# Performance work log

Measured on AMD Instinct MI355X. Metric: run time of the kernel, lower is better.

Reference implementation:

```python
import jax, jax.numpy as jnp
from jax import lax
import numpy as np

B, C_IN, C_OUT, H, W = 4, 256, 256, 64, 64
P = 4
DM = C_IN // P            # 64, d_model per parallel chunk
D_STATE = 16
D_CONV = 4
EXPAND = 2
D_INNER = EXPAND * DM     # 128
DT_RANK = max(1, -(-DM // 16))  # ceil(64/16) = 4


def setup_inputs() -> dict:
    key = jax.random.key(0)
    ks = jax.random.split(key, 12)
    s = lambda k, shape, scale=0.02: (jax.random.normal(k, shape, jnp.float32) * scale)
    dt = jax.random.uniform(ks[5], (D_INNER,), jnp.float32, 1e-3, 0.1)
    dt_bias = jnp.log(jnp.expm1(dt))  # inverse softplus, as in mamba_ssm init
    A_log = jnp.log(jnp.tile(jnp.arange(1, D_STATE + 1, dtype=jnp.float32), (D_INNER, 1)))
    return {
        "x": jax.random.normal(ks[0], (B, C_IN, H, W), jnp.float32),
        "ln_g": jnp.ones((C_IN,), jnp.float32),
        "ln_b": jnp.zeros((C_IN,), jnp.float32),
        "in_proj_w": s(ks[1], (2 * D_INNER, DM)),
        "conv_w": s(ks[2], (D_INNER, D_CONV), 0.1),
        "conv_b": jnp.zeros((D_INNER,), jnp.float32),
        "x_proj_w": s(ks[3], (DT_RANK + 2 * D_STATE, D_INNER)),
        "dt_proj_w": s(ks[4], (D_INNER, DT_RANK), 0.1),
        "dt_proj_b": dt_bias,
        "A_log": A_log,
        "D": jnp.ones((D_INNER,), jnp.float32),
        "out_proj_w": s(ks[6], (DM, D_INNER)),
        "skip_scale": jnp.ones((1,), jnp.float32),
        "proj_w": s(ks[7], (C_OUT, C_IN)),
        "proj_b": jnp.zeros((C_OUT,), jnp.float32),
        "cdc_w": s(ks[8], (C_OUT, 1, 3, 3), 0.1),      # depthwise 3x3, groups=C_OUT
        "theta_w": jnp.zeros((1, C_OUT), jnp.float32),  # nn.init.constant_(weight, 0)
        "theta_b": jnp.full((1,), -2.0, jnp.float32),   # nn.init.constant_(bias, -2)
        "pw_w": s(ks[9], (C_OUT, C_OUT)),               # 1x1 pointwise conv, no bias
    }


def _layernorm(x, g, b, eps=1e-5):
    mu = x.mean(-1, keepdims=True)
    var = ((x - mu) ** 2).mean(-1, keepdims=True)
    return (x - mu) * lax.rsqrt(var + eps) * g + b


def _mamba(x, in_proj_w, conv_w, conv_b, x_proj_w, dt_proj_w, dt_proj_b, A_log, D, out_proj_w):
    # x: [Bm, L, DM]
    xz = jnp.einsum('bld,ed->ble', x, in_proj_w)          # [Bm, L, 2*D_INNER]
    xc, z = jnp.split(xz, 2, axis=-1)
    # causal depthwise conv1d along L
    xt = jnp.swapaxes(xc, 1, 2)                           # [Bm, D_INNER, L]
    xt = lax.conv_general_dilated(xt, conv_w[:, None, :], (1,), [(D_CONV - 1, 0)],
                                  dimension_numbers=('NCH', 'OIH', 'NCH'),
                                  feature_group_count=D_INNER)
    xt = xt + conv_b[None, :, None]
    xs = jax.nn.silu(jnp.swapaxes(xt, 1, 2))              # [Bm, L, D_INNER]
    x_dbl = jnp.einsum('bld,ed->ble', xs, x_proj_w)       # [Bm, L, DT_RANK+2*D_STATE]
    dt, Bmat, Cmat = jnp.split(x_dbl, [DT_RANK, DT_RANK + D_STATE], axis=-1)
    delta = jax.nn.softplus(jnp.einsum('blr,dr->bld', dt, dt_proj_w) + dt_proj_b)
    A = -jnp.exp(A_log)                                   # [D_INNER, D_STATE]

    def step(h, inp):
        d_t, b_t, c_t, u_t = inp                          # [Bm,di],[Bm,ds],[Bm,ds],[Bm,di]
        h = h * jnp.exp(d_t[..., None] * A) + (d_t * u_t)[..., None] * b_t[:, None, :]
        return h, jnp.einsum('bds,bs->bd', h, c_t)

    h0 = jnp.zeros((x.shape[0], D_INNER, D_STATE), x.dtype)
    xs_t = (jnp.swapaxes(delta, 0, 1), jnp.swapaxes(Bmat, 0, 1),
            jnp.swapaxes(Cmat, 0, 1), jnp.swapaxes(xs, 0, 1))
    _, ys = lax.scan(step, h0, xs_t)                      # ys: [L, Bm, D_INNER]
    y = jnp.swapaxes(ys, 0, 1) + xs * D
    y = y * jax.nn.silu(z)
    return jnp.einsum('bld,od->blo', y, out_proj_w)       # [Bm, L, DM]


def reference(x, ln_g, ln_b, in_proj_w, conv_w, conv_b, x_proj_w, dt_proj_w, dt_proj_b,
              A_log, D, out_proj_w, skip_scale, proj_w, proj_b, cdc_w, theta_w, theta_b, pw_w):
    Bb, C = x.shape[:2]
    Hh, Ww = x.shape[2], x.shape[3]
    L = Hh * Ww
    x_flat = jnp.swapaxes(x.reshape(Bb, C, L), 1, 2)      # [B, L, C]
    x_norm = _layernorm(x_flat, ln_g, ln_b)
    # chunk along channel dim into P pieces, run shared Mamba on all as one big batch
    xc = jnp.moveaxis(x_norm.reshape(Bb, L, P, DM), 2, 0).reshape(P * Bb, L, DM)
    ym = _mamba(xc, in_proj_w, conv_w, conv_b, x_proj_w, dt_proj_w, dt_proj_b,
                A_log, D, out_proj_w) + skip_scale * xc
    ym = jnp.moveaxis(ym.reshape(P, Bb, L, DM), 0, 2).reshape(Bb, L, C)
    ym = _layernorm(ym, ln_g, ln_b)                       # same norm params (shared)
    yp = jnp.einsum('blc,oc->blo', ym, proj_w) + proj_b
    out = jnp.swapaxes(yp, 1, 2).reshape(Bb, C_OUT, Hh, Ww)
    # A_CDC: depthwise 3x3 conv + central-difference term
    out_normal = lax.conv_general_dilated(out, cdc_w, (1, 1), [(1, 1), (1, 1)],
                                          dimension_numbers=('NCHW', 'OIHW', 'NCHW'),
                                          feature_group_count=C_OUT)
    ksum = cdc_w.sum(axis=(2, 3))[:, 0]                   # [C_OUT]; depthwise 1x1 == scale
    edge = out_normal - out * ksum[None, :, None, None]
    theta = jax.nn.sigmoid(jnp.einsum('bchw,oc->bohw', out, theta_w)
                           + theta_b[None, :, None, None])
    cdc_out = out_normal + theta * edge
    g = jax.nn.gelu(cdc_out, approximate=False)           # nn.GELU exact
    cnn_out = jnp.einsum('bchw,oc->bohw', g, pw_w)        # 1x1 conv, no bias
    return out + cnn_out
```

## Files before the change

kernel.cpp:

```cpp
#include <hip/hip_runtime.h>
#include <hip/hip_bf16.h>
#include <math.h>

typedef __hip_bfloat16 bf16;
typedef short bf8_t __attribute__((ext_vector_type(8)));
typedef float f4_t  __attribute__((ext_vector_type(4)));
typedef float f2_t  __attribute__((ext_vector_type(2)));
#define MFMA16(a,b,c) __builtin_amdgcn_mfma_f32_16x16x32_bf16(a,b,c,0,0,0)
#define DEV __device__ __forceinline__

DEV float bf2f(bf16 h){ return __bfloat162float(h); }
DEV bf16 f2bf(float f){ return __float2bfloat16(f); }
DEV float ld(const void* p, size_t i, int md){
  return md ? ((const float*)p)[i] : bf2f(((const bf16*)p)[i]);
}
DEV float wred(float v){
  #pragma unroll
  for(int off=32; off>0; off>>=1) v += __shfl_down(v, off, 64);
  return __shfl(v, 0, 64);
}

__global__ __launch_bounds__(256) void k_detect(const unsigned short* __restrict__ xr, int* __restrict__ flag){
  __shared__ float sm[4];
  int t = threadIdx.x;
  float m = 0.f;
  for(int i=t;i<8192;i+=256){
    unsigned int w = ((unsigned int)xr[i]) << 16;
    float v = fabsf(__uint_as_float(w));
    if(v != v) v = 1e30f;
    m = fmaxf(m, v);
  }
  #pragma unroll
  for(int off=32; off>0; off>>=1) m = fmaxf(m, __shfl_down(m, off, 64));
  if((t & 63) == 0) sm[t >> 6] = m;
  __syncthreads();
  if(t == 0){
    float mm = fmaxf(fmaxf(sm[0], sm[1]), fmaxf(sm[2], sm[3]));
    *flag = (mm > 1e10f) ? 1 : 0;
  }
}

__global__ __launch_bounds__(256) void k_wcvt(const void* __restrict__ inw, const void* __restrict__ outw,
                                              const void* __restrict__ projw, const void* __restrict__ pww,
                                              bf16* __restrict__ dst, const int* __restrict__ modep){
  const int md = *modep;
  int g = blockIdx.x*256 + threadIdx.x;
  if(g >= 155648) return;
  const void* src; int i;
  if(g < 16384){ src = inw;   i = g; }
  else if(g < 24576){ src = outw;  i = g - 16384; }
  else if(g < 90112){ src = projw; i = g - 24576; }
  else { src = pww; i = g - 90112; }
  dst[g] = f2bf(ld(src, (size_t)i, md));
}

__global__ __launch_bounds__(256) void k_ln1(const void* __restrict__ x, const void* __restrict__ gam,
                                             const void* __restrict__ bet, bf16* __restrict__ xnb,
                                             const int* __restrict__ modep){
  __shared__ float sh[64*257];
  __shared__ float mus[64], rss[64];
  const int md = *modep;
  int t = threadIdx.x;
  int b = blockIdx.x >> 6, lt = blockIdx.x & 63;
  int l0 = lt << 6;
  int lane = t & 63, cg = t >> 6;
  size_t xbase = ((size_t)b << 20) + l0 + lane;
  if(md){
    const float* xp = (const float*)x + xbase;
    #pragma unroll 8
    for(int c = cg; c < 256; c += 4)
      sh[lane*257 + c] = xp[(size_t)c << 12];
  } else {
    const bf16* xp = (const bf16*)x + xbase;
    #pragma unroll 8
    for(int c = cg; c < 256; c += 4)
      sh[lane*257 + c] = bf2f(xp[(size_t)c << 12]);
  }
  __syncthreads();
  {
    int row = t >> 2, q = t & 3;
    const float* rp = sh + row*257 + q*64;
    float s = 0.f, s2 = 0.f;
    #pragma unroll 8
    for(int i=0;i<64;i++){ float v = rp[i]; s += v; s2 += v*v; }
    s  += __shfl_xor(s, 1, 64);  s2 += __shfl_xor(s2, 1, 64);
    s  += __shfl_xor(s, 2, 64);  s2 += __shfl_xor(s2, 2, 64);
    if(q == 0){
      float mu = s*(1.f/256.f);
      mus[row] = mu;
      rss[row] = rsqrtf(s2*(1.f/256.f) - mu*mu + 1e-5f);
    }
  }
  __syncthreads();
  int r0 = (t >> 6) << 4;
  #pragma unroll
  for(int k=0;k<4;k++){
    int c = (t & 63) + (k << 6);
    float gv = ld(gam, c, md), bv = ld(bet, c, md);
    #pragma unroll 4
    for(int rr=0; rr<16; rr++){
      int row = r0 + rr;
      xnb[((size_t)(b*4096 + l0 + row))*256 + c] =
        f2bf((sh[row*257 + c] - mus[row])*rss[row]*gv + bv);
    }
  }
}

__global__ __launch_bounds__(256) void k_inproj(const bf16* __restrict__ xnb, const bf16* __restrict__ wb,
                                                bf16* __restrict__ xcb, bf16* __restrict__ zb){
  __shared__ bf16 As[64*72];
  __shared__ bf16 Ws[256*72];
  int t = threadIdx.x;
  int bm = blockIdx.x >> 6, lt = blockIdx.x & 63;
  int p = bm >> 2, b = bm & 3, l0 = lt << 6;
  #pragma unroll
  for(int pass=0; pass<2; pass++){
    int idx = t + pass*256, r = idx >> 3, ch = idx & 7;
    *(uint4*)&As[r*72 + ch*8] = *(const uint4*)&xnb[((size_t)(b*4096 + l0 + r))*256 + p*64 + ch*8];
  }
  #pragma unroll
  for(int pass=0; pass<8; pass++){
    int idx = t + pass*256, e = idx >> 3, ch = idx & 7;
    *(uint4*)&Ws[e*72 + ch*8] = *(const uint4*)&wb[(size_t)e*64 + ch*8];
  }
  __syncthreads();
  int lane = t & 63, w = t >> 6, quad = lane >> 4, lr = lane & 15;
  f4_t acc[16];
  #pragma unroll
  for(int nt=0;nt<16;nt++) acc[nt] = (f4_t){0.f,0.f,0.f,0.f};
  #pragma unroll
  for(int kk=0; kk<64; kk+=32){
    bf8_t a = *(const bf8_t*)&As[(w*16 + lr)*72 + kk + quad*8];
    #pragma unroll
    for(int nt=0;nt<16;nt++){
      bf8_t bb = *(const bf8_t*)&Ws[(nt*16 + lr)*72 + kk + quad*8];
      acc[nt] = MFMA16(a, bb, acc[nt]);
    }
  }
  __syncthreads();
  bf16* Sl = Ws;
  #pragma unroll
  for(int nt=0;nt<16;nt++)
    #pragma unroll
    for(int r=0;r<4;r++)
      Sl[(w*16 + quad*4 + r)*264 + nt*16 + lr] = f2bf(acc[nt][r]);
  __syncthreads();
  #pragma unroll
  for(int pass=0; pass<8; pass++){
    int idx = t + pass*256, l = idx >> 5, c16 = idx & 31;
    int e0 = c16*8;
    uint4 v = *(uint4*)&Sl[l*264 + e0];
    size_t row = (size_t)bm*4096 + l0 + l;
    if(e0 < 128) *(uint4*)&xcb[row*128 + e0] = v;
    else         *(uint4*)&zb[row*128 + e0 - 128] = v;
  }
}

__global__ __launch_bounds__(256) void k_conv(const bf16* __restrict__ xcb, const void* __restrict__ cw,
                                              const void* __restrict__ cb, bf16* __restrict__ xsb,
                                              const int* __restrict__ modep){
  const int md = *modep;
  int g = blockIdx.x*256 + threadIdx.x;
  int d = g & 127;
  int t4 = g >> 7;
  int l4 = t4 & 1023;
  int bm = t4 >> 10;
  int l0 = l4 << 2;
  size_t base = ((size_t)bm*4096 + l0)*128 + d;
  const bf16* p = xcb + base;
  float w0 = ld(cw,(size_t)(d<<2)+0,md), w1 = ld(cw,(size_t)(d<<2)+1,md);
  float w2 = ld(cw,(size_t)(d<<2)+2,md), w3 = ld(cw,(size_t)(d<<2)+3,md);
  float bv = ld(cb,(size_t)d,md);
  float xm3, xm2, xm1;
  if(l4 > 0){ xm3 = bf2f(p[-384]); xm2 = bf2f(p[-256]); xm1 = bf2f(p[-128]); }
  else      { xm3 = 0.f; xm2 = 0.f; xm1 = 0.f; }
  float x0 = bf2f(p[0]), x1 = bf2f(p[128]), x2 = bf2f(p[256]), x3 = bf2f(p[384]);
  float y0 = fmaf(w0,xm3, fmaf(w1,xm2, fmaf(w2,xm1, fmaf(w3,x0, bv))));
  float y1 = fmaf(w0,xm2, fmaf(w1,xm1, fmaf(w2,x0,  fmaf(w3,x1, bv))));
  float y2 = fmaf(w0,xm1, fmaf(w1,x0,  fmaf(w2,x1,  fmaf(w3,x2, bv))));
  float y3 = fmaf(w0,x0,  fmaf(w1,x1,  fmaf(w2,x2,  fmaf(w3,x3, bv))));
  bf16* o = xsb + base;
  o[0]   = f2bf(y0 / (1.f + __expf(-y0)));
  o[128] = f2bf(y1 / (1.f + __expf(-y1)));
  o[256] = f2bf(y2 / (1.f + __expf(-y2)));
  o[384] = f2bf(y3 / (1.f + __expf(-y3)));
}

__global__ __launch_bounds__(256) void k_xproj(const bf16* __restrict__ xsb, const void* __restrict__ w,
                                               float* __restrict__ xdbl, const int* __restrict__ modep){
  __shared__ float At[128*68];
  __shared__ float Ww[128*40];
  const int md = *modep;
  int t = threadIdx.x;
  int bm = blockIdx.x >> 6, lt = blockIdx.x & 63, l0 = lt << 6;
  for(int idx = t; idx < 4608; idx += 256){
    int e = idx >> 7, k = idx & 127;
    Ww[k*40 + e] = ld(w, idx, md);
  }
  for(int idx = t; idx < 8192; idx += 256){
    int l = idx >> 7, k = idx & 127;
    At[k*68 + l] = bf2f(xsb[((size_t)bm*4096 + l0 + l)*128 + k]);
  }
  __syncthreads();
  int l = t & 63, eg = t >> 6;
  float acc[9] = {};
  for(int k=0;k<128;k++){
    float a = At[k*68 + l];
    #pragma unroll
    for(int j=0;j<9;j++) acc[j] = fmaf(a, Ww[k*40 + eg*9 + j], acc[j]);
  }
  float* o = xdbl + ((size_t)bm*4096 + l0 + l)*36 + eg*9;
  #pragma unroll
  for(int j=0;j<9;j++) o[j] = acc[j];
}

#define PTREE2(P, e1) \
  float e2s=(e1)*(e1), e4s=e2s*e2s, e8s=e4s*e4s; \
  f2_t P##0={(e1),e2s}; \
  f2_t P##1=P##0*(f2_t){e2s,e2s}; \
  f2_t e4v_={e4s,e4s}; f2_t P##2=P##0*e4v_, P##3=P##1*e4v_; \
  f2_t e8v_={e8s,e8s}; f2_t P##4=P##0*e8v_, P##5=P##1*e8v_, P##6=P##2*e8v_, P##7=P##3*e8v_;

__global__ __launch_bounds__(128) void k_scan1(const bf16* __restrict__ xsb, const float* __restrict__ xdbl,
                                               const void* __restrict__ dtw, const void* __restrict__ dtb,
                                               const void* __restrict__ Alog,
                                               float* __restrict__ CP, bf16* __restrict__ CSb,
                                               const int* __restrict__ modep){
  __shared__ float sh[32*36];
  __shared__ bf16 su[32*128];
  const int md = *modep;
  int d = threadIdx.x;
  int bm = blockIdx.x >> 7, c = blockIdx.x & 127;
  size_t row0 = (size_t)bm*4096 + (c<<5);
  {
    const float4* src = (const float4*)(xdbl + row0*36);
    for(int idx = d; idx < 288; idx += 128) ((float4*)sh)[idx] = src[idx];
    const uint4* gu = (const uint4*)(xsb + row0*128);
    uint4* lu = (uint4*)su;
    #pragma unroll
    for(int j=0;j<4;j++) lu[d + j*128] = gu[d + j*128];
  }
  float A[16];
  #pragma unroll
  for(int s=0;s<16;s++) A[s] = -expf(ld(Alog, (size_t)((d<<4)+s), md));
  float A0 = A[0];
  int fastf = 1;
  #pragma unroll
  for(int s=0;s<16;s++){
    float n = (float)(s+1);
    if(fabsf(A[s] - n*A0) > 2e-3f*fabsf(n*A0)) fastf = 0;
  }
  fastf = __all(fastf);
  float wdt[4];
  #pragma unroll
  for(int j=0;j<4;j++) wdt[j] = ld(dtw, (size_t)((d<<2)+j), md);
  float bdt = ld(dtb, (size_t)d, md);
  __syncthreads();
  f2_t h2[8];
  #pragma unroll
  for(int j=0;j<8;j++) h2[j] = (f2_t){0.f,0.f};
  float sumd = 0.f;
  if(fastf){
    #pragma unroll
    for(int tt=0;tt<32;tt++){
      const float* r = sh + tt*36;
      float4 dt4 = *(const float4*)r;
      float v = fmaf(dt4.x,wdt[0], fmaf(dt4.y,wdt[1], fmaf(dt4.z,wdt[2], fmaf(dt4.w,wdt[3], bdt))));
      float dv = fmaxf(v,0.f) + __logf(1.f + __expf(-fabsf(v)));
      float u = bf2f(su[tt*128 + d]);
      float du = dv*u; sumd += dv;
      const f2_t* B2 = (const f2_t*)(r+4);
      float e1 = __expf(dv*A0);
      PTREE2(p, e1);
      f2_t du2 = {du,du};
      h2[0] = h2[0]*p0 + du2*B2[0];
      h2[1] = h2[1]*p1 + du2*B2[1];
      h2[2] = h2[2]*p2 + du2*B2[2];
      h2[3] = h2[3]*p3 + du2*B2[3];
      h2[4] = h2[4]*p4 + du2*B2[4];
      h2[5] = h2[5]*p5 + du2*B2[5];
      h2[6] = h2[6]*p6 + du2*B2[6];
      h2[7] = h2[7]*p7 + du2*B2[7];
    }
  } else {
    for(int tt=0;tt<32;tt++){
      const float* r = sh + tt*36;
      float4 dt4 = *(const float4*)r;
      float v = fmaf(dt4.x,wdt[0], fmaf(dt4.y,wdt[1], fmaf(dt4.z,wdt[2], fmaf(dt4.w,wdt[3], bdt))));
      float dv = fmaxf(v,0.f) + __logf(1.f + __expf(-fabsf(v)));
      float u = bf2f(su[tt*128 + d]);
      float du = dv*u; sumd += dv;
      const float* Bp = r + 4;
      #pragma unroll
      for(int j=0;j<8;j++){
        f2_t e = { __expf(dv*A[2*j]), __expf(dv*A[2*j+1]) };
        f2_t bb = { Bp[2*j], Bp[2*j+1] };
        h2[j] = h2[j]*e + (f2_t){du,du}*bb;
      }
    }
  }
  size_t ob = ((size_t)(bm*128 + c)*128 + d) << 4;
  if(fastf){
    float qv = __expf(sumd*A0);
    PTREE2(P, qv);
    *(f2_t*)&CP[ob+ 0]=P0; *(f2_t*)&CP[ob+ 2]=P1; *(f2_t*)&CP[ob+ 4]=P2; *(f2_t*)&CP[ob+ 6]=P3;
    *(f2_t*)&CP[ob+ 8]=P4; *(f2_t*)&CP[ob+10]=P5; *(f2_t*)&CP[ob+12]=P6; *(f2_t*)&CP[ob+14]=P7;
  } else {
    #pragma unroll
    for(int s=0;s<16;s++) CP[ob+s] = __expf(sumd*A[s]);
  }
  __align__(16) bf16 pk[8];
  #pragma unroll
  for(int j=0;j<4;j++){ pk[2*j] = f2bf(h2[j].x); pk[2*j+1] = f2bf(h2[j].y); }
  *(uint4*)&CSb[ob] = *(uint4*)pk;
  #pragma unroll
  for(int j=0;j<4;j++){ pk[2*j] = f2bf(h2[4+j].x); pk[2*j+1] = f2bf(h2[4+j].y); }
  *(uint4*)&CSb[ob+8] = *(uint4*)pk;
}

__global__ __launch_bounds__(64) void k_scan2(float* __restrict__ CP, const bf16* __restrict__ CSb){
  int g = blockIdx.x*64 + threadIdx.x;
  int bm = g >> 11, ds = g & 2047;
  size_t base = ((size_t)bm << 18) + ds;
  float Pb[8], Sb[8];
  #pragma unroll
  for(int j=0;j<8;j++){
    size_t idx = base + ((size_t)j << 11);
    Pb[j] = CP[idx]; Sb[j] = bf2f(CSb[idx]);
  }
  float h = 0.f;
  #pragma unroll
  for(int grp=0; grp<16; grp++){
    float Pc[8], Sc[8];
    #pragma unroll
    for(int j=0;j<8;j++){ Pc[j]=Pb[j]; Sc[j]=Sb[j]; }
    if(grp < 15){
      #pragma unroll
      for(int j=0;j<8;j++){
        size_t idx = base + ((size_t)((grp+1)*8 + j) << 11);
        Pb[j] = CP[idx]; Sb[j] = bf2f(CSb[idx]);
      }
    }
    #pragma unroll
    for(int j=0;j<8;j++){
      size_t idx = base + ((size_t)(grp*8 + j) << 11);
      CP[idx] = h;
      h = fmaf(Pc[j], h, Sc[j]);
    }
  }
}

__global__ __launch_bounds__(128) void k_scan3(bf16* __restrict__ zb, const bf16* __restrict__ xsb,
                                               const float* __restrict__ xdbl,
                                               const void* __restrict__ dtw, const void* __restrict__ dtb,
                                               const void* __restrict__ Alog, const void* __restrict__ Dw,
                                               const float* __restrict__ CP, const int* __restrict__ modep){
  __shared__ float sh[32*36];
  __shared__ bf16 su[32*128];
  const int md = *modep;
  int d = threadIdx.x;
  int bm = blockIdx.x >> 7, c = blockIdx.x & 127;
  size_t row0 = (size_t)bm*4096 + (c<<5);
  {
    const float4* src = (const float4*)(xdbl + row0*36);
    for(int idx = d; idx < 288; idx += 128) ((float4*)sh)[idx] = src[idx];
    const uint4* gu = (const uint4*)(xsb + row0*128);
    uint4* lu = (uint4*)su;
    #pragma unroll
    for(int j=0;j<4;j++) lu[d + j*128] = gu[d + j*128];
  }
  float A[16];
  #pragma unroll
  for(int s=0;s<16;s++) A[s] = -expf(ld(Alog, (size_t)((d<<4)+s), md));
  float A0 = A[0];
  int fastf = 1;
  #pragma unroll
  for(int s=0;s<16;s++){
    float n = (float)(s+1);
    if(fabsf(A[s] - n*A0) > 2e-3f*fabsf(n*A0)) fastf = 0;
  }
  fastf = __all(fastf);
  float wdt[4];
  #pragma unroll
  for(int j=0;j<4;j++) wdt[j] = ld(dtw, (size_t)((d<<2)+j), md);
  float bdt = ld(dtb, (size_t)d, md);
  float Dd = ld(Dw, (size_t)d, md);
  size_t hb = ((size_t)(bm*128 + c)*128 + d) << 4;
  f2_t h2[8];
  #pragma unroll
  for(int j=0;j<8;j++) h2[j] = *(const f2_t*)&CP[hb + 2*j];
  __syncthreads();
  if(fastf){
    #pragma unroll
    for(int tt=0;tt<32;tt++){
      const float* r = sh + tt*36;
      size_t bg = (row0 + tt)*128 + d;
      float zv = bf2f(zb[bg]);
      float4 dt4 = *(const float4*)r;
      float v = fmaf(dt4.x,wdt[0], fmaf(dt4.y,wdt[1], fmaf(dt4.z,wdt[2], fmaf(dt4.w,wdt[3], bdt))));
      float dv = fmaxf(v,0.f) + __logf(1.f + __expf(-fabsf(v)));
      float u  = bf2f(su[tt*128 + d]);
      float du = dv*u;
      const f2_t* B2 = (const f2_t*)(r+4);
      const f2_t* C2 = (const f2_t*)(r+20);
      float e1 = __expf(dv*A0);
      PTREE2(p, e1);
      f2_t du2 = {du,du};
      f2_t ya = {0.f,0.f}, yb = {0.f,0.f};
      h2[0] = h2[0]*p0 + du2*B2[0];  ya += h2[0]*C2[0];
      h2[1] = h2[1]*p1 + du2*B2[1];  yb += h2[1]*C2[1];
      h2[2] = h2[2]*p2 + du2*B2[2];  ya += h2[2]*C2[2];
      h2[3] = h2[3]*p3 + du2*B2[3];  yb += h2[3]*C2[3];
      h2[4] = h2[4]*p4 + du2*B2[4];  ya += h2[4]*C2[4];
      h2[5] = h2[5]*p5 + du2*B2[5];  yb += h2[5]*C2[5];
      h2[6] = h2[6]*p6 + du2*B2[6];  ya += h2[6]*C2[6];
      h2[7] = h2[7]*p7 + du2*B2[7];  yb += h2[7]*C2[7];
      float y = (ya.x + ya.y) + (yb.x + yb.y);
      float yv = (y + u*Dd) * (zv / (1.f + __expf(-zv)));
      zb[bg] = f2bf(yv);
    }
  } else {
    for(int tt=0;tt<32;tt++){
      const float* r = sh + tt*36;
      size_t bg = (row0 + tt)*128 + d;
      float zv = bf2f(zb[bg]);
      float4 dt4 = *(const float4*)r;
      float v = fmaf(dt4.x,wdt[0], fmaf(dt4.y,wdt[1], fmaf(dt4.z,wdt[2], fmaf(dt4.w,wdt[3], bdt))));
      float dv = fmaxf(v,0.f) + __logf(1.f + __expf(-fabsf(v)));
      float u  = bf2f(su[tt*128 + d]);
      float du = dv*u;
      const float* Bp = r + 4;
      const float* Cp = r + 20;
      f2_t ya = {0.f,0.f};
      #pragma unroll
      for(int j=0;j<8;j++){
        f2_t e = { __expf(dv*A[2*j]), __expf(dv*A[2*j+1]) };
        f2_t bb = { Bp[2*j], Bp[2*j+1] };
        f2_t cc = { Cp[2*j], Cp[2*j+1] };
        h2[j] = h2[j]*e + (f2_t){du,du}*bb;
        ya += h2[j]*cc;
      }
      float y = ya.x + ya.y;
      float yv = (y + u*Dd) * (zv / (1.f + __expf(-zv)));
      zb[bg] = f2bf(yv);
    }
  }
}

__global__ __launch_bounds__(256) void k_outproj(const bf16* __restrict__ yb, const bf16* __restrict__ xnb,
                                                 const bf16* __restrict__ wb, const void* __restrict__ ss,
                                                 bf16* __restrict__ ymb, const int* __restrict__ modep){
  __shared__ bf16 As[64*72];
  __shared__ bf16 Ws[64*72];
  const int md = *modep;
  int t = threadIdx.x;
  int bm = blockIdx.x >> 6, lt = blockIdx.x & 63;
  int p = bm >> 2, b = bm & 3, l0 = lt << 6;
  int lane = t & 63, w = t >> 6, quad = lane >> 4, lr = lane & 15;
  f4_t acc[4];
  #pragma unroll
  for(int nt=0;nt<4;nt++) acc[nt] = (f4_t){0.f,0.f,0.f,0.f};
  for(int kb=0; kb<2; kb++){
    if(kb) __syncthreads();
    int k0 = kb << 6;
    #pragma unroll
    for(int pass=0; pass<2; pass++){
      int idx = t + pass*256, r = idx >> 3, ch = idx & 7;
      *(uint4*)&As[r*72 + ch*8] = *(const uint4*)&yb[((size_t)bm*4096 + l0 + r)*128 + k0 + ch*8];
    }
    #pragma unroll
    for(int pass=0; pass<2; pass++){
      int idx = t + pass*256, o = idx >> 3, ch = idx & 7;
      *(uint4*)&Ws[o*72 + ch*8] = *(const uint4*)&wb[(size_t)o*128 + k0 + ch*8];
    }
    __syncthreads();
    #pragma unroll
    for(int kk=0; kk<64; kk+=32){
      bf8_t a = *(const bf8_t*)&As[(w*16 + lr)*72 + kk + quad*8];
      #pragma unroll
      for(int nt=0;nt<4;nt++){
        bf8_t bb = *(const bf8_t*)&Ws[(nt*16 + lr)*72 + kk + quad*8];
        acc[nt] = MFMA16(a, bb, acc[nt]);
      }
    }
  }
  __syncthreads();
  bf16* Sl = As;
  #pragma unroll
  for(int nt=0;nt<4;nt++)
    #pragma unroll
    for(int r=0;r<4;r++)
      Sl[(w*16 + quad*4 + r)*72 + nt*16 + lr] = f2bf(acc[nt][r]);
  __syncthreads();
  float sv = ld(ss, 0, md);
  #pragma unroll
  for(int pass=0; pass<2; pass++){
    int idx = t + pass*256, l = idx >> 3, ch = idx & 7;
    size_t gi = ((size_t)b*4096 + l0 + l)*256 + p*64 + ch*8;
    uint4 yv = *(uint4*)&Sl[l*72 + ch*8];
    uint4 xv = *(const uint4*)&xnb[gi];
    const bf16* y8 = (const bf16*)&yv;
    const bf16* x8 = (const bf16*)&xv;
    uint4 ov; bf16* o8 = (bf16*)&ov;
    #pragma unroll
    for(int j=0;j<8;j++) o8[j] = f2bf(fmaf(sv, bf2f(x8[j]), bf2f(y8[j])));
    *(uint4*)&ymb[gi] = ov;
  }
}

__global__ __launch_bounds__(256) void k_ln2(bf16* __restrict__ ymb, const void* __restrict__ gam,
                                             const void* __restrict__ bet, const int* __restrict__ modep){
  const int md = *modep;
  int lane = threadIdx.x & 63, wv = threadIdx.x >> 6;
  size_t row = (size_t)blockIdx.x*4 + wv;
  bf16* rp = ymb + row*256 + (lane<<2);
  __align__(8) bf16 raw[4];
  *(ushort4*)raw = *(const ushort4*)rp;
  float v[4];
  #pragma unroll
  for(int i=0;i<4;i++) v[i] = bf2f(raw[i]);
  float s = v[0]+v[1]+v[2]+v[3];
  float s2 = v[0]*v[0]+v[1]*v[1]+v[2]*v[2]+v[3]*v[3];
  s = wred(s); s2 = wred(s2);
  float mu = s*(1.f/256.f);
  float rs = rsqrtf(s2*(1.f/256.f) - mu*mu + 1e-5f);
  int c = lane << 2;
  #pragma unroll
  for(int i=0;i<4;i++) raw[i] = f2bf((v[i]-mu)*rs*ld(gam,c+i,md) + ld(bet,c+i,md));
  *(ushort4*)rp = *(ushort4*)raw;
}

__global__ __launch_bounds__(256) void k_proj(const bf16* __restrict__ ymb, const bf16* __restrict__ wb,
                                              const void* __restrict__ pb, bf16* __restrict__ outbb,
                                              const void* __restrict__ tw, const void* __restrict__ tb2,
                                              float* __restrict__ theta, const int* __restrict__ modep){
  __shared__ bf16 As[64*72];
  __shared__ bf16 Ws[256*72];
  const int md = *modep;
  int t = threadIdx.x;
  int row0 = blockIdx.x << 6;
  int b = row0 >> 12, l0 = row0 & 4095;
  int lane = t & 63, w = t >> 6, quad = lane >> 4, lr = lane & 15;
  f4_t acc[16];
  #pragma unroll
  for(int nt=0;nt<16;nt++) acc[nt] = (f4_t){0.f,0.f,0.f,0.f};
  for(int kb=0; kb<4; kb++){
    if(kb) __syncthreads();
    int k0 = kb << 6;
    #pragma unroll
    for(int pass=0; pass<2; pass++){
      int idx = t + pass*256, r = idx >> 3, ch = idx & 7;
      *(uint4*)&As[r*72 + ch*8] = *(const uint4*)&ymb[((size_t)(row0 + r))*256 + k0 + ch*8];
    }
    #pragma unroll
    for(int pass=0; pass<8; pass++){
      int idx = t + pass*256, e = idx >> 3, ch = idx & 7;
      *(uint4*)&Ws[e*72 + ch*8] = *(const uint4*)&wb[(size_t)e*256 + k0 + ch*8];
    }
    __syncthreads();
    #pragma unroll
    for(int kk=0; kk<64; kk+=32){
      bf8_t a = *(const bf8_t*)&As[(w*16 + lr)*72 + kk + quad*8];
      #pragma unroll
      for(int nt=0;nt<16;nt++){
        bf8_t bb = *(const bf8_t*)&Ws[(nt*16 + lr)*72 + kk + quad*8];
        acc[nt] = MFMA16(a, bb, acc[nt]);
      }
    }
  }
  __syncthreads();
  bf16* Sl = Ws;
  #pragma unroll
  for(int nt=0;nt<16;nt++){
    float bv = ld(pb, nt*16 + lr, md);
    #pragma unroll
    for(int r=0;r<4;r++)
      Sl[(nt*16 + lr)*72 + w*16 + quad*4 + r] = f2bf(acc[nt][r] + bv);
  }
  __syncthreads();
  #pragma unroll
  for(int pass=0; pass<8; pass++){
    int idx = t + pass*256, o = idx >> 3, ch = idx & 7;
    uint4 v = *(uint4*)&Sl[o*72 + ch*8];
    *(uint4*)&outbb[((size_t)(b*256 + o) << 12) + l0 + ch*8] = v;
  }
  if(t < 64){
    float acc2 = 0.f;
    #pragma unroll 8
    for(int o=0;o<256;o++)
      acc2 = fmaf(bf2f(Sl[o*72 + t]), ld(tw, (size_t)o, md), acc2);
    float v = acc2 + ld(tb2, 0, md);
    theta[((size_t)b << 12) + l0 + t] = 1.f / (1.f + __expf(-v));
  }
}

__global__ __launch_bounds__(256) void k_cdc(const bf16* __restrict__ outbb, const float* __restrict__ theta,
                                             const void* __restrict__ cw, bf16* __restrict__ gbufb,
                                             const int* __restrict__ modep){
  const int md = *modep;
  int g = blockIdx.x*256 + threadIdx.x;
  int w4 = g & 15;
  int h0 = (g >> 4) & 63;
  int c  = (g >> 10) & 255;
  int b  = g >> 18;
  int w0 = w4 << 2;
  float wk[9]; float ks = 0.f;
  #pragma unroll
  for(int j=0;j<9;j++){ wk[j] = ld(cw, (size_t)c*9 + j, md); ks += wk[j]; }
  const bf16* base = outbb + (((size_t)b*256 + c) << 12);
  float X[3][6];
  #pragma unroll
  for(int dy=0;dy<3;dy++){
    int hh = h0 + dy - 1;
    #pragma unroll
    for(int dx=0;dx<6;dx++){
      int ww = w0 + dx - 1;
      X[dy][dx] = (hh>=0 && hh<64 && ww>=0 && ww<64) ? bf2f(base[(hh<<6)+ww]) : 0.f;
    }
  }
  float4 th = *(const float4*)&theta[((size_t)b<<12) + (h0<<6) + w0];
  float thv[4] = {th.x, th.y, th.z, th.w};
  __align__(8) bf16 outp[4];
  #pragma unroll
  for(int k=0;k<4;k++){
    float on = 0.f;
    #pragma unroll
    for(int dy=0;dy<3;dy++)
      #pragma unroll
      for(int dx=0;dx<3;dx++)
        on = fmaf(X[dy][k+dx], wk[dy*3+dx], on);
    float ctr  = X[1][k+1];
    float edge = on - ctr*ks;
    float cd   = fmaf(thv[k], edge, on);
    outp[k] = f2bf(0.5f * cd * (1.f + erff(cd * 0.70710678118654752f)));
  }
  *(ushort4*)&gbufb[(((size_t)b*256 + c) << 12) + (h0<<6) + w0] = *(ushort4*)outp;
}

__global__ __launch_bounds__(256) void k_pw(const bf16* __restrict__ gbufb, const bf16* __restrict__ outbb,
                                            const bf16* __restrict__ wb, void* __restrict__ outp,
                                            const int* __restrict__ modep){
  __shared__ bf16 As[64*72];
  __shared__ bf16 Bs[256*72];
  const int md = *modep;
  int t = threadIdx.x;
  int b  = blockIdx.x >> 6;
  int ot = (blockIdx.x >> 4) & 3;
  int ht = blockIdx.x & 15;
  int o0 = ot << 6, hw0 = ht << 8;
  int lane = t & 63, w = t >> 6, quad = lane >> 4, lr = lane & 15;
  f4_t acc[16];
  #pragma unroll
  for(int nt=0;nt<16;nt++) acc[nt] = (f4_t){0.f,0.f,0.f,0.f};
  for(int kb=0; kb<4; kb++){
    if(kb) __syncthreads();
    int k0 = kb << 6;
    #pragma unroll
    for(int pass=0; pass<2; pass++){
      int idx = t + pass*256, r = idx >> 3, ch = idx & 7;
      *(uint4*)&As[r*72 + ch*8] = *(const uint4*)&wb[(size_t)(o0 + r)*256 + k0 + ch*8];
    }
    #pragma unroll
    for(int pass=0; pass<8; pass++){
      int idx = t + pass*256, cc = idx >> 5, hc = idx & 31;
      uint4 gv = *(const uint4*)&gbufb[((size_t)(b*256 + k0 + cc) << 12) + hw0 + hc*8];
      const bf16* g8 = (const bf16*)&gv;
      #pragma unroll
      for(int j=0;j<8;j++) Bs[(hc*8 + j)*72 + cc] = g8[j];
    }
    __syncthreads();
    #pragma unroll
    for(int kk=0; kk<64; kk+=32){
      bf8_t a = *(const bf8_t*)&As[(w*16 + lr)*72 + kk + quad*8];
      #pragma unroll
      for(int nt=0;nt<16;nt++){
        bf8_t bb = *(const bf8_t*)&Bs[(nt*16 + lr)*72 + kk + quad*8];
        acc[nt] = MFMA16(a, bb, acc[nt]);
      }
    }
  }
  __syncthreads();
  bf16* Sl = Bs;
  #pragma unroll
  for(int nt=0;nt<16;nt++)
    #pragma unroll
    for(int r=0;r<4;r++)
      Sl[(w*16 + quad*4 + r)*264 + nt*16 + lr] = f2bf(acc[nt][r]);
  __syncthreads();
  #pragma unroll
  for(int pass=0; pass<8; pass++){
    int idx = t + pass*256, ol = idx >> 5, c16 = idx & 31;
    size_t ro = ((size_t)(b*256 + o0 + ol) << 12) + hw0 + c16*8;
    uint4 sv = *(uint4*)&Sl[ol*264 + c16*8];
    uint4 rv = *(const uint4*)&outbb[ro];
    const bf16* s8 = (const bf16*)&sv;
    const bf16* r8 = (const bf16*)&rv;
    if(md){
      float4 f0, f1;
      f0.x = bf2f(s8[0]) + bf2f(r8[0]); f0.y = bf2f(s8[1]) + bf2f(r8[1]);
      f0.z = bf2f(s8[2]) + bf2f(r8[2]); f0.w = bf2f(s8[3]) + bf2f(r8[3]);
      f1.x = bf2f(s8[4]) + bf2f(r8[4]); f1.y = bf2f(s8[5]) + bf2f(r8[5]);
      f1.z = bf2f(s8[6]) + bf2f(r8[6]); f1.w = bf2f(s8[7]) + bf2f(r8[7]);
      *(float4*)&((float*)outp)[ro]     = f0;
      *(float4*)&((float*)outp)[ro + 4] = f1;
    } else {
      uint4 ov; bf16* o8 = (bf16*)&ov;
      #pragma unroll
      for(int j=0;j<8;j++) o8[j] = f2bf(bf2f(s8[j]) + bf2f(r8[j]));
      *(uint4*)&((bf16*)outp)[ro] = ov;
    }
  }
}

extern "C" void kernel_launch(void* const* d_in, const int* in_sizes, int n_in,
                              void* d_out, int out_size, void* d_ws, size_t ws_size,
                              hipStream_t stream){
  const void* x      = d_in[0];
  const void* ln_g   = d_in[1];
  const void* ln_b   = d_in[2];
  const void* inw    = d_in[3];
  const void* convw  = d_in[4];
  const void* convb  = d_in[5];
  const void* xpw    = d_in[6];
  const void* dtw    = d_in[7];
  const void* dtb    = d_in[8];
  const void* Alog   = d_in[9];
  const void* Dw     = d_in[10];
  const void* outw   = d_in[11];
  const void* sscale = d_in[12];
  const void* projw  = d_in[13];
  const void* projb  = d_in[14];
  const void* cdcw   = d_in[15];
  const void* thw    = d_in[16];
  const void* thb    = d_in[17];
  const void* pww    = d_in[18];
  float* ws = (float*)d_ws;

  bf16*  xnb   = (bf16*)(ws);
  bf16*  xcb   = (bf16*)(ws + 2097152);
  float* CP    = ws + 2097152;
  bf16*  ymb   = (bf16*)(ws + 2097152);
  bf16*  outbb = (bf16*)(ws + 4194304);
  bf16*  zb    = (bf16*)(ws + 6291456);
  bf16*  gbufb = (bf16*)(ws + 6291456);
  bf16*  xsb   = (bf16*)(ws + 10485760);
  float* theta = ws + 10485760;
  float* xdbl  = ws + 14680064;
  int*   flag  = (int*)(ws + 17039360);
  bf16*  wsb   = (bf16*)(ws + 17039364);
  bf16*  inwb  = wsb;
  bf16*  outwb = wsb + 16384;
  bf16*  projwb= wsb + 24576;
  bf16*  pwwb  = wsb + 90112;
  bf16*  CSb   = (bf16*)d_out;

  k_detect <<<1,    256, 0, stream>>>((const unsigned short*)x, flag);
  k_wcvt   <<<608,  256, 0, stream>>>(inw, outw, projw, pww, wsb, flag);
  k_ln1    <<<256,  256, 0, stream>>>(x, ln_g, ln_b, xnb, flag);
  k_inproj <<<1024, 256, 0, stream>>>(xnb, inwb, xcb, zb);
  k_conv   <<<8192, 256, 0, stream>>>(xcb, convw, convb, xsb, flag);
  k_xproj  <<<1024, 256, 0, stream>>>(xsb, xpw, xdbl, flag);
  k_scan1  <<<2048, 128, 0, stream>>>(xsb, xdbl, dtw, dtb, Alog, CP, CSb, flag);
  k_scan2  <<<512,  64,  0, stream>>>(CP, CSb);
  k_scan3  <<<2048, 128, 0, stream>>>(zb, xsb, xdbl, dtw, dtb, Alog, Dw, CP, flag);
  k_outproj<<<1024, 256, 0, stream>>>(zb, xnb, outwb, sscale, ymb, flag);
  k_ln2    <<<4096, 256, 0, stream>>>(ymb, ln_g, ln_b, flag);
  k_proj   <<<256,  256, 0, stream>>>(ymb, projwb, projb, outbb, thw, thb, theta, flag);
  k_cdc    <<<4096, 256, 0, stream>>>(outbb, theta, cdcw, gbufb, flag);
  k_pw     <<<256,  256, 0, stream>>>(gbufb, outbb, pwwb, d_out, flag);
}
```

Measured before the change: 357.4 us.

## Fuse x_proj into scan chunk pass using MFMA bf16 matmul

```diff
diff --git a/kernel.cpp b/kernel.cpp
--- a/kernel.cpp
+++ b/kernel.cpp
@@ -186,34 +186,6 @@
   o[384] = f2bf(y3 / (1.f + __expf(-y3)));
 }
 
-__global__ __launch_bounds__(256) void k_xproj(const bf16* __restrict__ xsb, const void* __restrict__ w,
-                                               float* __restrict__ xdbl, const int* __restrict__ modep){
-  __shared__ float At[128*68];
-  __shared__ float Ww[128*40];
-  const int md = *modep;
-  int t = threadIdx.x;
-  int bm = blockIdx.x >> 6, lt = blockIdx.x & 63, l0 = lt << 6;
-  for(int idx = t; idx < 4608; idx += 256){
-    int e = idx >> 7, k = idx & 127;
-    Ww[k*40 + e] = ld(w, idx, md);
-  }
-  for(int idx = t; idx < 8192; idx += 256){
-    int l = idx >> 7, k = idx & 127;
-    At[k*68 + l] = bf2f(xsb[((size_t)bm*4096 + l0 + l)*128 + k]);
-  }
-  __syncthreads();
-  int l = t & 63, eg = t >> 6;
-  float acc[9] = {};
-  for(int k=0;k<128;k++){
-    float a = At[k*68 + l];
-    #pragma unroll
-    for(int j=0;j<9;j++) acc[j] = fmaf(a, Ww[k*40 + eg*9 + j], acc[j]);
-  }
-  float* o = xdbl + ((size_t)bm*4096 + l0 + l)*36 + eg*9;
-  #pragma unroll
-  for(int j=0;j<9;j++) o[j] = acc[j];
-}
-
 #define PTREE2(P, e1) \
   float e2s=(e1)*(e1), e4s=e2s*e2s, e8s=e4s*e4s; \
   f2_t P##0={(e1),e2s}; \
@@ -221,25 +193,57 @@
   f2_t e4v_={e4s,e4s}; f2_t P##2=P##0*e4v_, P##3=P##1*e4v_; \
   f2_t e8v_={e8s,e8s}; f2_t P##4=P##0*e8v_, P##5=P##1*e8v_, P##6=P##2*e8v_, P##7=P##3*e8v_;
 
-__global__ __launch_bounds__(128) void k_scan1(const bf16* __restrict__ xsb, const float* __restrict__ xdbl,
-                                               const void* __restrict__ dtw, const void* __restrict__ dtb,
-                                               const void* __restrict__ Alog,
-                                               float* __restrict__ CP, bf16* __restrict__ CSb,
-                                               const int* __restrict__ modep){
-  __shared__ float sh[32*36];
-  __shared__ bf16 su[32*128];
-  const int md = *modep;
-  int d = threadIdx.x;
-  int bm = blockIdx.x >> 7, c = blockIdx.x & 127;
-  size_t row0 = (size_t)bm*4096 + (c<<5);
-  {
-    const float4* src = (const float4*)(xdbl + row0*36);
-    for(int idx = d; idx < 288; idx += 128) ((float4*)sh)[idx] = src[idx];
-    const uint4* gu = (const uint4*)(xsb + row0*128);
-    uint4* lu = (uint4*)su;
-    #pragma unroll
-    for(int j=0;j<4;j++) lu[d + j*128] = gu[d + j*128];
-  }
+__global__ __launch_bounds__(256) void k_cxs1(const bf16* __restrict__ xsb, const void* __restrict__ xpw,
+                                              float* __restrict__ xdbl,
+                                              const void* __restrict__ dtw, const void* __restrict__ dtb,
+                                              const void* __restrict__ Alog,
+                                              float* __restrict__ CP, bf16* __restrict__ CSb,
+                                              const int* __restrict__ modep){
+  __shared__ bf16 As[64*136];
+  __shared__ bf16 Ws[64*136];
+  float* sh = (float*)Ws;
+  const int md = *modep;
+  int t = threadIdx.x;
+  int bm = blockIdx.x >> 6, lt = blockIdx.x & 63;
+  size_t row0g = (size_t)bm*4096 + (lt << 6);
+  #pragma unroll
+  for(int pass=0; pass<4; pass++){
+    int idx = t + pass*256, r = idx >> 4, ch = idx & 15;
+    *(uint4*)&As[r*136 + ch*8] = *(const uint4*)&xsb[(row0g + r)*128 + ch*8];
+  }
+  for(int idx = t; idx < 8192; idx += 256){
+    int e = idx >> 7, k = idx & 127;
+    Ws[e*136 + k] = (e < 36) ? f2bf(ld(xpw, (size_t)e*128 + k, md)) : f2bf(0.f);
+  }
+  __syncthreads();
+  int lane = t & 63, w = t >> 6, quad = lane >> 4, lr = lane & 15;
+  f4_t acc[3];
+  #pragma unroll
+  for(int nt=0;nt<3;nt++) acc[nt] = (f4_t){0.f,0.f,0.f,0.f};
+  #pragma unroll
+  for(int kk=0; kk<128; kk+=32){
+    bf8_t a = *(const bf8_t*)&As[(w*16 + lr)*136 + kk + quad*8];
+    #pragma unroll
+    for(int nt=0;nt<3;nt++){
+      bf8_t bb = *(const bf8_t*)&Ws[(nt*16 + lr)*136 + kk + quad*8];
+      acc[nt] = MFMA16(a, bb, acc[nt]);
+    }
+  }
+  __syncthreads();
+  #pragma unroll
+  for(int nt=0;nt<3;nt++){
+    int e = nt*16 + lr;
+    if(e < 36){
+      #pragma unroll
+      for(int r=0;r<4;r++){
+        int row = w*16 + quad*4 + r;
+        float v = acc[nt][r];
+        sh[row*36 + e] = v;
+        xdbl[(row0g + row)*36 + e] = v;
+      }
+    }
+  }
+  int d = t & 127, chunk = t >> 7;
   float A[16];
   #pragma unroll
   for(int s=0;s<16;s++) A[s] = -expf(ld(Alog, (size_t)((d<<4)+s), md));
@@ -260,14 +264,16 @@
   #pragma unroll
   for(int j=0;j<8;j++) h2[j] = (f2_t){0.f,0.f};
   float sumd = 0.f;
+  const float* shc = sh + chunk*32*36;
+  const bf16* uc = As + chunk*32*136;
   if(fastf){
     #pragma unroll
     for(int tt=0;tt<32;tt++){
-      const float* r = sh + tt*36;
+      const float* r = shc + tt*36;
       float4 dt4 = *(const float4*)r;
       float v = fmaf(dt4.x,wdt[0], fmaf(dt4.y,wdt[1], fmaf(dt4.z,wdt[2], fmaf(dt4.w,wdt[3], bdt))));
       float dv = fmaxf(v,0.f) + __logf(1.f + __expf(-fabsf(v)));
-      float u = bf2f(su[tt*128 + d]);
+      float u = bf2f(uc[tt*136 + d]);
       float du = dv*u; sumd += dv;
       const f2_t* B2 = (const f2_t*)(r+4);
       float e1 = __expf(dv*A0);
@@ -284,11 +290,11 @@
     }
   } else {
     for(int tt=0;tt<32;tt++){
-      const float* r = sh + tt*36;
+      const float* r = shc + tt*36;
       float4 dt4 = *(const float4*)r;
       float v = fmaf(dt4.x,wdt[0], fmaf(dt4.y,wdt[1], fmaf(dt4.z,wdt[2], fmaf(dt4.w,wdt[3], bdt))));
       float dv = fmaxf(v,0.f) + __logf(1.f + __expf(-fabsf(v)));
-      float u = bf2f(su[tt*128 + d]);
+      float u = bf2f(uc[tt*136 + d]);
       float du = dv*u; sumd += dv;
       const float* Bp = r + 4;
       #pragma unroll
@@ -299,6 +305,7 @@
       }
     }
   }
+  int c = lt*2 + chunk;
   size_t ob = ((size_t)(bm*128 + c)*128 + d) << 4;
   if(fastf){
     float qv = __expf(sumd*A0);
@@ -759,8 +766,7 @@
   k_ln1    <<<256,  256, 0, stream>>>(x, ln_g, ln_b, xnb, flag);
   k_inproj <<<1024, 256, 0, stream>>>(xnb, inwb, xcb, zb);
   k_conv   <<<8192, 256, 0, stream>>>(xcb, convw, convb, xsb, flag);
-  k_xproj  <<<1024, 256, 0, stream>>>(xsb, xpw, xdbl, flag);
-  k_scan1  <<<2048, 128, 0, stream>>>(xsb, xdbl, dtw, dtb, Alog, CP, CSb, flag);
+  k_cxs1   <<<1024, 256, 0, stream>>>(xsb, xpw, xdbl, dtw, dtb, Alog, CP, CSb, flag);
   k_scan2  <<<512,  64,  0, stream>>>(CP, CSb);
   k_scan3  <<<2048, 128, 0, stream>>>(zb, xsb, xdbl, dtw, dtb, Alog, Dw, CP, flag);
   k_outproj<<<1024, 256, 0, stream>>>(zb, xnb, outwb, sscale, ymb, flag);
```

Result: faster. 334.6 us (-6.4%).
